# Optimization experiments

Hardware: AMD Instinct MI355X
Metric: run time of the kernel (lower is better)

The kernel has to match this reference:

```python
import math
import jax, jax.numpy as jnp
import numpy as np

B, S, H, E, F = 4, 2048, 1024, 8, 2048
CAPACITY_FACTOR = 1.25


def setup_inputs() -> dict:
    key = jax.random.key(0)
    ks = jax.random.split(key, 5)
    x = jax.random.normal(ks[0], (B, S, H), dtype=jnp.float32)
    gate_w = jax.random.normal(ks[1], (H, E), dtype=jnp.float32) * 0.02
    w1 = jax.random.normal(ks[2], (E, H, F), dtype=jnp.float32) * 0.02
    w2 = jax.random.normal(ks[3], (E, F, H), dtype=jnp.float32) * 0.02
    w3 = jax.random.normal(ks[4], (E, H, F), dtype=jnp.float32) * 0.02
    return {"x": x, "gate_w": gate_w, "w1": w1, "w2": w2, "w3": w3}


def reference(x, gate_w, w1, w2, w3):
    b, s, h = x.shape
    T = b * s
    e = gate_w.shape[1]
    xf = x.reshape(T, h)                           # [T, H]
    logits = xf @ gate_w                           # [T, E]
    capacity = min(math.ceil(T / e * CAPACITY_FACTOR), T)
    # Expert-choice: each expert picks its top-`capacity` tokens.
    scores, idx = jax.lax.top_k(logits.T, capacity)  # both [E, C]
    # Per-expert softmax over the selected tokens (dim=0 of the column vector in torch == capacity axis here).
    weights = jax.nn.softmax(scores, axis=1)       # [E, C]
    gathered = xf[idx]                             # [E, C, H]
    # Grouped SwiGLU FFN
    a = jnp.einsum('ech,ehf->ecf', gathered, w1)
    g = jnp.einsum('ech,ehf->ecf', gathered, w3)
    hidden = jax.nn.silu(a) * g                    # [E, C, F]
    out_e = jnp.einsum('ecf,efh->ech', hidden, w2) # [E, C, H]
    out_e = out_e * weights[..., None]
    # Weighted scatter-add combine
    yf = jnp.zeros((T, h), dtype=x.dtype).at[idx.reshape(-1)].add(
        out_e.reshape(-1, h))
    return yf.reshape(b, s, h), jnp.float32(0.0)
```

## Files before the change

### kernel.cpp

```cpp
#include <hip/hip_runtime.h>
#include <stdint.h>

typedef unsigned short ushort_t;
typedef __bf16 bf16x8 __attribute__((ext_vector_type(8)));
typedef float f32x4 __attribute__((ext_vector_type(4)));

#define T_TOK 8192
#define HDIM  1024
#define EXP   8
#define FDIM  2048
#define CAP   1280

__device__ __forceinline__ unsigned short f2b(float f) {
  unsigned u = __float_as_uint(f);
  u = (u + 0x7fffu + ((u >> 16) & 1u)) >> 16;
  return (unsigned short)u;
}

__device__ __forceinline__ unsigned pk2(unsigned short lo, unsigned short hi) {
  return (unsigned)lo | ((unsigned)hi << 16);
}

__device__ __forceinline__ void gl_lds16(const void* g, void* l) {
  __builtin_amdgcn_global_load_lds((__attribute__((address_space(1))) void*)g,
                                   (__attribute__((address_space(3))) void*)l,
                                   16, 0, 0);
}

__global__ void __launch_bounds__(256) gate_logits_k(
    const float* __restrict__ x, const float* __restrict__ gw,
    float* __restrict__ logits)
{
  int wave = threadIdx.x >> 6, lane = threadIdx.x & 63;
  int t = blockIdx.x * 4 + wave;
  const float* xr = x + (size_t)t * HDIM;
  float acc[8];
#pragma unroll
  for (int i = 0; i < 8; ++i) acc[i] = 0.f;
#pragma unroll
  for (int i = 0; i < 16; ++i) {
    int h = i * 64 + lane;
    float xv = xr[h];
    const float4* g4 = (const float4*)(gw + (size_t)h * EXP);
    float4 lo = g4[0], hi = g4[1];
    acc[0] += xv * lo.x; acc[1] += xv * lo.y; acc[2] += xv * lo.z; acc[3] += xv * lo.w;
    acc[4] += xv * hi.x; acc[5] += xv * hi.y; acc[6] += xv * hi.z; acc[7] += xv * hi.w;
  }
#pragma unroll
  for (int off = 32; off > 0; off >>= 1) {
#pragma unroll
    for (int i = 0; i < 8; ++i) acc[i] += __shfl_xor(acc[i], off, 64);
  }
  if (lane == 0) {
#pragma unroll
    for (int i = 0; i < 8; ++i) logits[(size_t)t * EXP + i] = acc[i];
  }
}

__device__ __forceinline__ float unmap_f(unsigned m) {
  unsigned u = (m & 0x80000000u) ? (m ^ 0x80000000u) : ~m;
  return __uint_as_float(u);
}

__global__ void __launch_bounds__(1024) topk_softmax_k(
    const float* __restrict__ logits, int* __restrict__ idxo, float* __restrict__ wgto)
{
  __shared__ unsigned long long keys[T_TOK];
  int e = blockIdx.x;
  int tid = threadIdx.x;
  for (int i = tid; i < T_TOK; i += 1024) {
    unsigned u = __float_as_uint(logits[(size_t)i * EXP + e]);
    unsigned m = (u & 0x80000000u) ? ~u : (u | 0x80000000u);
    keys[i] = ((unsigned long long)m << 32) | (unsigned)i;
  }
  __syncthreads();
  for (int k = 2; k <= T_TOK; k <<= 1) {
    for (int j = k >> 1; j > 0; j >>= 1) {
      for (int p = tid; p < T_TOK / 2; p += 1024) {
        int i = ((p & ~(j - 1)) << 1) | (p & (j - 1));
        int ixj = i | j;
        unsigned long long a = keys[i], b = keys[ixj];
        bool desc = ((i & k) == 0);
        if ((a < b) == desc) { keys[i] = b; keys[ixj] = a; }
      }
      __syncthreads();
    }
  }
  if (tid < 64) {
    float mx = unmap_f((unsigned)(keys[0] >> 32));
    float sum = 0.f;
    for (int c = tid; c < CAP; c += 64)
      sum += __expf(unmap_f((unsigned)(keys[c] >> 32)) - mx);
#pragma unroll
    for (int off = 32; off > 0; off >>= 1) sum += __shfl_xor(sum, off, 64);
    float inv = 1.f / sum;
    for (int c = tid; c < CAP; c += 64) {
      unsigned long long kk = keys[c];
      idxo[e * CAP + c] = (int)(kk & 0xffffffffull);
      wgto[e * CAP + c] = __expf(unmap_f((unsigned)(kk >> 32)) - mx) * inv;
    }
  }
}

__global__ void __launch_bounds__(256) cast_bf16_k(
    const float* __restrict__ x, ushort_t* __restrict__ xb)
{
  size_t base = ((size_t)blockIdx.x * 256 + threadIdx.x) * 8;
  float4 a = *(const float4*)(x + base);
  float4 b = *(const float4*)(x + base + 4);
  uint4 v;
  v.x = pk2(f2b(a.x), f2b(a.y)); v.y = pk2(f2b(a.z), f2b(a.w));
  v.z = pk2(f2b(b.x), f2b(b.y)); v.w = pk2(f2b(b.z), f2b(b.w));
  *(uint4*)(xb + base) = v;
}

__global__ void __launch_bounds__(256) transpose_cast_k(
    const float* __restrict__ in, ushort_t* __restrict__ out, int R, int Cc)
{
  __shared__ float tile[64][65];
  int tilesC = Cc >> 6;
  int tilesPer = (R >> 6) * tilesC;
  int b = blockIdx.x;
  int e = b / tilesPer;
  int tb = b - e * tilesPer;
  int rt = tb / tilesC, ct = tb - rt * tilesC;
  const float* src = in + (size_t)e * R * Cc;
  ushort_t* dst = out + (size_t)e * R * Cc;
  int tr = threadIdx.x >> 4, tc = threadIdx.x & 15;
#pragma unroll
  for (int it = 0; it < 4; ++it) {
    int r = (rt << 6) + (it << 4) + tr;
    int c = (ct << 6) + (tc << 2);
    float4 v = *(const float4*)(src + (size_t)r * Cc + c);
    tile[(it << 4) + tr][(tc << 2) + 0] = v.x;
    tile[(it << 4) + tr][(tc << 2) + 1] = v.y;
    tile[(it << 4) + tr][(tc << 2) + 2] = v.z;
    tile[(it << 4) + tr][(tc << 2) + 3] = v.w;
  }
  __syncthreads();
#pragma unroll
  for (int it = 0; it < 4; ++it) {
    int cl = (it << 4) + tr;
    int rl = tc << 2;
    unsigned lo = pk2(f2b(tile[rl + 0][cl]), f2b(tile[rl + 1][cl]));
    unsigned hi = pk2(f2b(tile[rl + 2][cl]), f2b(tile[rl + 3][cl]));
    unsigned long long v = (unsigned long long)lo | ((unsigned long long)hi << 32);
    *(unsigned long long*)(dst + (size_t)((ct << 6) + cl) * R + (rt << 6) + rl) = v;
  }
}

__global__ void __launch_bounds__(256) gemm1_swiglu_k(
    const ushort_t* __restrict__ xb,
    const ushort_t* __restrict__ w1t,
    const ushort_t* __restrict__ w3t,
    const int* __restrict__ idx,
    ushort_t* __restrict__ hidden)
{
  int b = blockIdx.x;
  int ni_ = b & 7; int t1 = b >> 3; int mt = t1 % 10; int t2 = t1 / 10;
  int ng = t2 & 3; int e = t2 >> 2;
  int nt = ng * 8 + ni_;

  __shared__ __bf16 Alds[128 * 32];
  __shared__ __bf16 B1lds[64 * 32];
  __shared__ __bf16 B3lds[64 * 32];

  int tid = threadIdx.x;
  int lane = tid & 63, wave = tid >> 6;
  int wm = wave & 1, wn = wave >> 1;
  int l15 = lane & 15, quad = lane >> 4;

  int r0 = tid >> 2, kc0 = tid & 3;
  int r1 = r0 + 64;
  const int* idxe = idx + e * CAP + mt * 128;
  const ushort_t* a0 = xb + (size_t)idxe[r0] * HDIM + kc0 * 8;
  const ushort_t* a1 = xb + (size_t)idxe[r1] * HDIM + kc0 * 8;
  const ushort_t* wb1 = w1t + ((size_t)e * FDIM + nt * 64) * HDIM;
  const ushort_t* wb3 = w3t + ((size_t)e * FDIM + nt * 64) * HDIM;
  const ushort_t* b1p = wb1 + (size_t)r0 * HDIM + kc0 * 8;
  const ushort_t* b3p = wb3 + (size_t)r0 * HDIM + kc0 * 8;

  f32x4 acc1[4][2];
  f32x4 acc3[4][2];
#pragma unroll
  for (int i = 0; i < 4; ++i)
#pragma unroll
    for (int j = 0; j < 2; ++j) {
      acc1[i][j] = (f32x4){0.f, 0.f, 0.f, 0.f};
      acc3[i][j] = (f32x4){0.f, 0.f, 0.f, 0.f};
    }

  for (int kt = 0; kt < HDIM / 32; ++kt) {
    gl_lds16(a0,  Alds  + (size_t)tid * 8);
    gl_lds16(a1,  Alds  + (size_t)(tid + 256) * 8);
    gl_lds16(b1p, B1lds + (size_t)tid * 8);
    gl_lds16(b3p, B3lds + (size_t)tid * 8);
    __syncthreads();

    bf16x8 af[4], bf1[2], bf3[2];
#pragma unroll
    for (int i = 0; i < 4; ++i)
      af[i]  = *(const bf16x8*)(Alds  + ((wm * 64 + i * 16 + l15) * 32 + quad * 8));
#pragma unroll
    for (int j = 0; j < 2; ++j) {
      bf1[j] = *(const bf16x8*)(B1lds + ((wn * 32 + j * 16 + l15) * 32 + quad * 8));
      bf3[j] = *(const bf16x8*)(B3lds + ((wn * 32 + j * 16 + l15) * 32 + quad * 8));
    }
#pragma unroll
    for (int mi = 0; mi < 4; ++mi)
#pragma unroll
      for (int nj = 0; nj < 2; ++nj) {
        acc1[mi][nj] = __builtin_amdgcn_mfma_f32_16x16x32_bf16(af[mi], bf1[nj], acc1[mi][nj], 0, 0, 0);
        acc3[mi][nj] = __builtin_amdgcn_mfma_f32_16x16x32_bf16(af[mi], bf3[nj], acc3[mi][nj], 0, 0, 0);
      }
    __syncthreads();
    a0 += 32; a1 += 32; b1p += 32; b3p += 32;
  }

  ushort_t* hb = hidden + ((size_t)e * CAP + mt * 128) * FDIM + nt * 64;
#pragma unroll
  for (int mi = 0; mi < 4; ++mi)
#pragma unroll
    for (int nj = 0; nj < 2; ++nj)
#pragma unroll
      for (int r = 0; r < 4; ++r) {
        int row = wm * 64 + mi * 16 + quad * 4 + r;
        int col = wn * 32 + nj * 16 + l15;
        float v1 = acc1[mi][nj][r];
        float v3 = acc3[mi][nj][r];
        float s = (v1 / (1.f + __expf(-v1))) * v3;
        hb[(size_t)row * FDIM + col] = f2b(s);
      }
}

__global__ void __launch_bounds__(256) gemm2_scatter_k(
    const ushort_t* __restrict__ hidden,
    const ushort_t* __restrict__ w2t,
    const int* __restrict__ idx,
    const float* __restrict__ wgt,
    float* __restrict__ y)
{
  int b = blockIdx.x;
  int nt = b & 7; int t1 = b >> 3; int mt = t1 % 10; int t2 = t1 / 10;
  int kk = t2 & 1; int e = t2 >> 1;

  __shared__ __bf16 Alds[128 * 32];
  __shared__ __bf16 Blds[128 * 32];
  __shared__ int   idxs[128];
  __shared__ float wgts[128];

  int tid = threadIdx.x;
  int lane = tid & 63, wave = tid >> 6;
  int wm = wave & 1, wn = wave >> 1;
  int l15 = lane & 15, quad = lane >> 4;

  if (tid < 128) {
    idxs[tid] = idx[e * CAP + mt * 128 + tid];
    wgts[tid] = wgt[e * CAP + mt * 128 + tid];
  }

  int r0 = tid >> 2, kc0 = tid & 3;
  int r1 = r0 + 64;
  size_t kof = (size_t)kk * (FDIM / 2);
  const ushort_t* a0 = hidden + ((size_t)e * CAP + mt * 128 + r0) * FDIM + kof + kc0 * 8;
  const ushort_t* a1 = hidden + ((size_t)e * CAP + mt * 128 + r1) * FDIM + kof + kc0 * 8;
  const ushort_t* b0 = w2t + ((size_t)e * HDIM + nt * 128 + r0) * FDIM + kof + kc0 * 8;
  const ushort_t* b1 = w2t + ((size_t)e * HDIM + nt * 128 + r1) * FDIM + kof + kc0 * 8;

  f32x4 acc[4][4];
#pragma unroll
  for (int i = 0; i < 4; ++i)
#pragma unroll
    for (int j = 0; j < 4; ++j) acc[i][j] = (f32x4){0.f, 0.f, 0.f, 0.f};

  for (int kt = 0; kt < (FDIM / 2) / 32; ++kt) {
    gl_lds16(a0, Alds + (size_t)tid * 8);
    gl_lds16(a1, Alds + (size_t)(tid + 256) * 8);
    gl_lds16(b0, Blds + (size_t)tid * 8);
    gl_lds16(b1, Blds + (size_t)(tid + 256) * 8);
    __syncthreads();

    bf16x8 af[4], bf[4];
#pragma unroll
    for (int i = 0; i < 4; ++i) {
      af[i] = *(const bf16x8*)(Alds + ((wm * 64 + i * 16 + l15) * 32 + quad * 8));
      bf[i] = *(const bf16x8*)(Blds + ((wn * 64 + i * 16 + l15) * 32 + quad * 8));
    }
#pragma unroll
    for (int mi = 0; mi < 4; ++mi)
#pragma unroll
      for (int nj = 0; nj < 4; ++nj)
        acc[mi][nj] = __builtin_amdgcn_mfma_f32_16x16x32_bf16(af[mi], bf[nj], acc[mi][nj], 0, 0, 0);
    __syncthreads();
    a0 += 32; a1 += 32; b0 += 32; b1 += 32;
  }

#pragma unroll
  for (int mi = 0; mi < 4; ++mi)
#pragma unroll
    for (int nj = 0; nj < 4; ++nj)
#pragma unroll
      for (int r = 0; r < 4; ++r) {
        int row = wm * 64 + mi * 16 + quad * 4 + r;
        int col = nt * 128 + wn * 64 + nj * 16 + l15;
        float v = acc[mi][nj][r] * wgts[row];
        atomicAdd(y + (size_t)idxs[row] * HDIM + col, v);
      }
}

extern "C" void kernel_launch(void* const* d_in, const int* in_sizes, int n_in,
                              void* d_out, int out_size, void* d_ws, size_t ws_size,
                              hipStream_t stream)
{
  const float* x  = (const float*)d_in[0];
  const float* gw = (const float*)d_in[1];
  const float* w1 = (const float*)d_in[2];
  const float* w2 = (const float*)d_in[3];
  const float* w3 = (const float*)d_in[4];
  float* y = (float*)d_out;

  char* ws = (char*)d_ws;
  float*    logits = (float*)(ws + 0x0);
  int*      idx    = (int*)(ws + 0x40000);
  float*    wgt    = (float*)(ws + 0x4A000);
  ushort_t* xb     = (ushort_t*)(ws + 0x54000);
  ushort_t* w1t    = (ushort_t*)(ws + 0x1054000);
  ushort_t* w3t    = (ushort_t*)(ws + 0x3054000);
  ushort_t* w2t    = (ushort_t*)(ws + 0x5054000);
  ushort_t* hid    = (ushort_t*)(ws + 0x7054000);

  hipMemsetAsync(d_out, 0, (size_t)out_size * sizeof(float), stream);
  gate_logits_k<<<T_TOK / 4, 256, 0, stream>>>(x, gw, logits);
  topk_softmax_k<<<EXP, 1024, 0, stream>>>(logits, idx, wgt);
  cast_bf16_k<<<T_TOK * HDIM / (256 * 8), 256, 0, stream>>>(x, xb);
  transpose_cast_k<<<EXP * (HDIM / 64) * (FDIM / 64), 256, 0, stream>>>(w1, w1t, HDIM, FDIM);
  transpose_cast_k<<<EXP * (HDIM / 64) * (FDIM / 64), 256, 0, stream>>>(w3, w3t, HDIM, FDIM);
  transpose_cast_k<<<EXP * (FDIM / 64) * (HDIM / 64), 256, 0, stream>>>(w2, w2t, FDIM, HDIM);
  gemm1_swiglu_k<<<EXP * 4 * 10 * 8, 256, 0, stream>>>(xb, w1t, w3t, idx, hid);
  gemm2_scatter_k<<<EXP * 2 * 10 * 8, 256, 0, stream>>>(hid, w2t, idx, wgt, y);
}
```

Before: 572.8 us.

## Replace bitonic-sort top-k with radix threshold select and fuse cast into gating

Replaces the per-expert full bitonic sort of 8192 keys, which runs in one 1024-thread block per expert, with a four-pass 8-bit radix histogram that finds the capacity threshold. A parallel emit kernel then compacts the selected tokens with ballot and atomics and accumulates the softmax denominators, and the final normalisation moves into the second GEMM. The bf16 cast of x is fused into the gate-logits kernel, which now writes logits transposed, and the three weight transposes are merged into one launch. Selected tokens now arrive in arbitrary order, and the sums built with atomics make the weights nondeterministic at the float-rounding level.

Result: slower. 604.8 us (+5.6%).

```diff
diff --git a/kernel.cpp b/kernel.cpp
--- a/kernel.cpp
+++ b/kernel.cpp
@@ -16,24 +16,31 @@
   u = (u + 0x7fffu + ((u >> 16) & 1u)) >> 16;
   return (unsigned short)u;
 }
-
 __device__ __forceinline__ unsigned pk2(unsigned short lo, unsigned short hi) {
   return (unsigned)lo | ((unsigned)hi << 16);
 }
-
+__device__ __forceinline__ unsigned map_u(float f) {
+  unsigned u = __float_as_uint(f);
+  return (u & 0x80000000u) ? ~u : (u | 0x80000000u);
+}
+__device__ __forceinline__ float unmap_f(unsigned m) {
+  unsigned u = (m & 0x80000000u) ? (m ^ 0x80000000u) : ~m;
+  return __uint_as_float(u);
+}
 __device__ __forceinline__ void gl_lds16(const void* g, void* l) {
   __builtin_amdgcn_global_load_lds((__attribute__((address_space(1))) void*)g,
                                    (__attribute__((address_space(3))) void*)l,
                                    16, 0, 0);
 }
 
-__global__ void __launch_bounds__(256) gate_logits_k(
+__global__ void __launch_bounds__(256) gate_cast_k(
     const float* __restrict__ x, const float* __restrict__ gw,
-    float* __restrict__ logits)
+    float* __restrict__ logitsT, ushort_t* __restrict__ xb)
 {
   int wave = threadIdx.x >> 6, lane = threadIdx.x & 63;
   int t = blockIdx.x * 4 + wave;
   const float* xr = x + (size_t)t * HDIM;
+  ushort_t* xbr = xb + (size_t)t * HDIM;
   float acc[8];
 #pragma unroll
   for (int i = 0; i < 8; ++i) acc[i] = 0.f;
@@ -41,6 +48,7 @@
   for (int i = 0; i < 16; ++i) {
     int h = i * 64 + lane;
     float xv = xr[h];
+    xbr[h] = f2b(xv);
     const float4* g4 = (const float4*)(gw + (size_t)h * EXP);
     float4 lo = g4[0], hi = g4[1];
     acc[0] += xv * lo.x; acc[1] += xv * lo.y; acc[2] += xv * lo.z; acc[3] += xv * lo.w;
@@ -53,74 +61,117 @@
   }
   if (lane == 0) {
 #pragma unroll
-    for (int i = 0; i < 8; ++i) logits[(size_t)t * EXP + i] = acc[i];
-  }
-}
-
-__device__ __forceinline__ float unmap_f(unsigned m) {
-  unsigned u = (m & 0x80000000u) ? (m ^ 0x80000000u) : ~m;
-  return __uint_as_float(u);
-}
-
-__global__ void __launch_bounds__(1024) topk_softmax_k(
-    const float* __restrict__ logits, int* __restrict__ idxo, float* __restrict__ wgto)
-{
-  __shared__ unsigned long long keys[T_TOK];
-  int e = blockIdx.x;
-  int tid = threadIdx.x;
-  for (int i = tid; i < T_TOK; i += 1024) {
-    unsigned u = __float_as_uint(logits[(size_t)i * EXP + e]);
-    unsigned m = (u & 0x80000000u) ? ~u : (u | 0x80000000u);
-    keys[i] = ((unsigned long long)m << 32) | (unsigned)i;
-  }
+    for (int i = 0; i < 8; ++i) logitsT[(size_t)i * T_TOK + t] = acc[i];
+  }
+}
+
+__global__ void __launch_bounds__(256) select_k(
+    const float* __restrict__ logitsT,
+    unsigned* __restrict__ thr, int* __restrict__ need, unsigned* __restrict__ umax)
+{
+  __shared__ int hist[256];
+  __shared__ unsigned s_pref, s_max;
+  __shared__ int s_rem;
+  int e = blockIdx.x, tid = threadIdx.x;
+  const float* base = logitsT + (size_t)e * T_TOK;
+
+  unsigned m[32];
+#pragma unroll
+  for (int i = 0; i < 32; ++i) m[i] = map_u(base[tid + i * 256]);
+
+  if (tid == 0) { s_pref = 0; s_rem = CAP; s_max = 0; }
   __syncthreads();
-  for (int k = 2; k <= T_TOK; k <<= 1) {
-    for (int j = k >> 1; j > 0; j >>= 1) {
-      for (int p = tid; p < T_TOK / 2; p += 1024) {
-        int i = ((p & ~(j - 1)) << 1) | (p & (j - 1));
-        int ixj = i | j;
-        unsigned long long a = keys[i], b = keys[ixj];
-        bool desc = ((i & k) == 0);
-        if ((a < b) == desc) { keys[i] = b; keys[ixj] = a; }
-      }
-      __syncthreads();
-    }
-  }
-  if (tid < 64) {
-    float mx = unmap_f((unsigned)(keys[0] >> 32));
-    float sum = 0.f;
-    for (int c = tid; c < CAP; c += 64)
-      sum += __expf(unmap_f((unsigned)(keys[c] >> 32)) - mx);
-#pragma unroll
-    for (int off = 32; off > 0; off >>= 1) sum += __shfl_xor(sum, off, 64);
-    float inv = 1.f / sum;
-    for (int c = tid; c < CAP; c += 64) {
-      unsigned long long kk = keys[c];
-      idxo[e * CAP + c] = (int)(kk & 0xffffffffull);
-      wgto[e * CAP + c] = __expf(unmap_f((unsigned)(kk >> 32)) - mx) * inv;
-    }
-  }
-}
-
-__global__ void __launch_bounds__(256) cast_bf16_k(
-    const float* __restrict__ x, ushort_t* __restrict__ xb)
-{
-  size_t base = ((size_t)blockIdx.x * 256 + threadIdx.x) * 8;
-  float4 a = *(const float4*)(x + base);
-  float4 b = *(const float4*)(x + base + 4);
-  uint4 v;
-  v.x = pk2(f2b(a.x), f2b(a.y)); v.y = pk2(f2b(a.z), f2b(a.w));
-  v.z = pk2(f2b(b.x), f2b(b.y)); v.w = pk2(f2b(b.z), f2b(b.w));
-  *(uint4*)(xb + base) = v;
-}
-
-__global__ void __launch_bounds__(256) transpose_cast_k(
-    const float* __restrict__ in, ushort_t* __restrict__ out, int R, int Cc)
+
+  for (int r = 0; r < 4; ++r) {
+    hist[tid] = 0;
+    __syncthreads();
+    unsigned pref = s_pref;
+    int shift = 24 - 8 * r, hi = 32 - 8 * r;
+#pragma unroll
+    for (int i = 0; i < 32; ++i) {
+      unsigned u = m[i];
+      if (r == 0) {
+        atomicMax(&s_max, u);
+        atomicAdd(&hist[u >> 24], 1);
+      } else if ((u >> hi) == (pref >> hi)) {
+        atomicAdd(&hist[(u >> shift) & 255], 1);
+      }
+    }
+    __syncthreads();
+    if (tid == 0) {
+      int rem = s_rem, acc = 0, b;
+      for (b = 255; b >= 0; --b) {
+        int c = hist[b];
+        if (acc + c >= rem) break;
+        acc += c;
+      }
+      s_pref = pref | ((unsigned)b << shift);
+      s_rem = rem - acc;
+    }
+    __syncthreads();
+  }
+  if (tid == 0) {
+    thr[e] = s_pref;
+    need[e] = s_rem;
+    umax[e] = s_max;
+  }
+}
+
+__global__ void __launch_bounds__(256) emit_k(
+    const float* __restrict__ logitsT,
+    const unsigned* __restrict__ thr, const int* __restrict__ need,
+    const unsigned* __restrict__ umax,
+    int* __restrict__ idxo, float* __restrict__ exo,
+    int* __restrict__ cnt, int* __restrict__ tie, float* __restrict__ expsum)
+{
+  int t = blockIdx.x * 256 + threadIdx.x;
+  int lane = threadIdx.x & 63;
+#pragma unroll
+  for (int e = 0; e < EXP; ++e) {
+    float f = logitsT[(size_t)e * T_TOK + t];
+    unsigned u = map_u(f);
+    unsigned te = thr[e];
+    float fm = unmap_f(umax[e]);
+    float v = __expf(f - fm);
+    bool sel = u > te;
+    unsigned long long mask = __ballot(sel);
+    int nsel = __popcll(mask);
+    int base = 0;
+    if (lane == 0 && nsel) base = atomicAdd(&cnt[e], nsel);
+    base = __shfl(base, 0, 64);
+    if (sel) {
+      int slot = base + __popcll(mask & ((1ull << lane) - 1ull));
+      idxo[e * CAP + slot] = t;
+      exo[e * CAP + slot] = v;
+    }
+    float vs = sel ? v : 0.f;
+#pragma unroll
+    for (int off = 32; off > 0; off >>= 1) vs += __shfl_xor(vs, off, 64);
+    if (lane == 0 && vs != 0.f) atomicAdd(&expsum[e], vs);
+    if (u == te) {
+      int k = atomicAdd(&tie[e], 1);
+      if (k < need[e]) {
+        int slot = atomicAdd(&cnt[e], 1);
+        idxo[e * CAP + slot] = t;
+        exo[e * CAP + slot] = v;
+        atomicAdd(&expsum[e], v);
+      }
+    }
+  }
+}
+
+__global__ void __launch_bounds__(256) transpose3_k(
+    const float* __restrict__ w1, const float* __restrict__ w3, const float* __restrict__ w2,
+    ushort_t* __restrict__ w1t, ushort_t* __restrict__ w3t, ushort_t* __restrict__ w2t)
 {
   __shared__ float tile[64][65];
+  int b = blockIdx.x;
+  const float* in; ushort_t* out; int R, Cc;
+  if (b < 4096)      { in = w1; out = w1t; R = HDIM; Cc = FDIM; }
+  else if (b < 8192) { in = w3; out = w3t; R = HDIM; Cc = FDIM; b -= 4096; }
+  else               { in = w2; out = w2t; R = FDIM; Cc = HDIM; b -= 8192; }
   int tilesC = Cc >> 6;
   int tilesPer = (R >> 6) * tilesC;
-  int b = blockIdx.x;
   int e = b / tilesPer;
   int tb = b - e * tilesPer;
   int rt = tb / tilesC, ct = tb - rt * tilesC;
@@ -237,7 +288,7 @@
     const ushort_t* __restrict__ hidden,
     const ushort_t* __restrict__ w2t,
     const int* __restrict__ idx,
-    const float* __restrict__ wgt,
+    const float* __restrict__ ex, const float* __restrict__ expsum,
     float* __restrict__ y)
 {
   int b = blockIdx.x;
@@ -256,7 +307,7 @@
 
   if (tid < 128) {
     idxs[tid] = idx[e * CAP + mt * 128 + tid];
-    wgts[tid] = wgt[e * CAP + mt * 128 + tid];
+    wgts[tid] = ex[e * CAP + mt * 128 + tid] / expsum[e];
   }
 
   int r0 = tid >> 2, kc0 = tid & 3;
@@ -320,22 +371,27 @@
   float* y = (float*)d_out;
 
   char* ws = (char*)d_ws;
-  float*    logits = (float*)(ws + 0x0);
-  int*      idx    = (int*)(ws + 0x40000);
-  float*    wgt    = (float*)(ws + 0x4A000);
-  ushort_t* xb     = (ushort_t*)(ws + 0x54000);
-  ushort_t* w1t    = (ushort_t*)(ws + 0x1054000);
-  ushort_t* w3t    = (ushort_t*)(ws + 0x3054000);
-  ushort_t* w2t    = (ushort_t*)(ws + 0x5054000);
-  ushort_t* hid    = (ushort_t*)(ws + 0x7054000);
+  float*    logitsT = (float*)(ws + 0x0);
+  int*      idx     = (int*)(ws + 0x40000);
+  float*    exo     = (float*)(ws + 0x4A000);
+  unsigned* thr    = (unsigned*)(ws + 0x54000);
+  int*      need   = (int*)(ws + 0x54020);
+  unsigned* umax   = (unsigned*)(ws + 0x54040);
+  int*      cnt    = (int*)(ws + 0x54060);
+  int*      tie    = (int*)(ws + 0x54080);
+  float*    expsum = (float*)(ws + 0x540A0);
+  ushort_t* xb     = (ushort_t*)(ws + 0x60000);
+  ushort_t* w1t    = (ushort_t*)(ws + 0x1060000);
+  ushort_t* w3t    = (ushort_t*)(ws + 0x3060000);
+  ushort_t* w2t    = (ushort_t*)(ws + 0x5060000);
+  ushort_t* hid    = (ushort_t*)(ws + 0x7060000);
 
   hipMemsetAsync(d_out, 0, (size_t)out_size * sizeof(float), stream);
-  gate_logits_k<<<T_TOK / 4, 256, 0, stream>>>(x, gw, logits);
-  topk_softmax_k<<<EXP, 1024, 0, stream>>>(logits, idx, wgt);
-  cast_bf16_k<<<T_TOK * HDIM / (256 * 8), 256, 0, stream>>>(x, xb);
-  transpose_cast_k<<<EXP * (HDIM / 64) * (FDIM / 64), 256, 0, stream>>>(w1, w1t, HDIM, FDIM);
-  transpose_cast_k<<<EXP * (HDIM / 64) * (FDIM / 64), 256, 0, stream>>>(w3, w3t, HDIM, FDIM);
-  transpose_cast_k<<<EXP * (FDIM / 64) * (HDIM / 64), 256, 0, stream>>>(w2, w2t, FDIM, HDIM);
+  hipMemsetAsync(ws + 0x54000, 0, 256, stream);
+  gate_cast_k<<<T_TOK / 4, 256, 0, stream>>>(x, gw, logitsT, xb);
+  select_k<<<EXP, 256, 0, stream>>>(logitsT, thr, need, umax);
+  emit_k<<<T_TOK / 256, 256, 0, stream>>>(logitsT, thr, need, umax, idx, exo, cnt, tie, expsum);
+  transpose3_k<<<3 * 4096, 256, 0, stream>>>(w1, w3, w2, w1t, w3t, w2t);
   gemm1_swiglu_k<<<EXP * 4 * 10 * 8, 256, 0, stream>>>(xb, w1t, w3t, idx, hid);
-  gemm2_scatter_k<<<EXP * 2 * 10 * 8, 256, 0, stream>>>(hid, w2t, idx, wgt, y);
-}
+  gemm2_scatter_k<<<EXP * 2 * 10 * 8, 256, 0, stream>>>(hid, w2t, idx, exo, expsum, y);
+}
```
